# Performance work log

Hardware: AMD Instinct MI355X
Metric: run time of the kernel (lower is better)

The kernel has to match this reference:

```python
import jax, jax.numpy as jnp
import numpy as np

MARGIN = 0.5
ALPHA = 1.0
BETA = 0.5
TEMP = 0.07
TEMP_MIN = 0.01
TEMP_MAX = 0.5
STEP = 1  # step_count after first forward (buffer starts at 0, incremented before use)
WARMUP = 1000


def _l2norm(x):
    return x / jnp.maximum(jnp.linalg.norm(x, axis=1, keepdims=True), 1e-12)


def _adaptive_temp(std):
    return jnp.clip(TEMP * (1.0 + std), TEMP_MIN, TEMP_MAX)


def setup_inputs() -> dict:
    key = jax.random.key(0)
    k1, k2, k3, k4, k5 = jax.random.split(key, 5)
    B, D, C, P = 4096, 1024, 1000, 2000
    return {
        "features": jax.random.normal(k1, (B, D), dtype=jnp.float32),
        "cur_proto": jax.random.normal(k2, (C, D), dtype=jnp.float32),
        "prev_proto": jax.random.normal(k3, (P, D), dtype=jnp.float32),
        "labels": jax.random.randint(k4, (B,), 0, C, dtype=jnp.int32),
        "prev_proto_labels": jax.random.randint(k5, (P,), 0, C, dtype=jnp.int32),
    }


def reference(features, cur_proto, prev_proto, labels, prev_proto_labels):
    # With randn protos, proto norms ~ sqrt(D)=32 in (1e-3, 100), so valid_mask
    # is all-True; the per-sample torch loop vectorizes exactly.
    f = _l2norm(features)          # [B, D]
    cp = _l2norm(cur_proto)        # [C, D]

    # --- positive alignment: cosine_embedding_loss(target=1) = mean(1 - cos) ---
    pos_cos = jnp.sum(f * cp[labels], axis=1)       # [B]
    pos_loss = jnp.mean(1.0 - pos_cos)

    # --- curriculum weight at step 1 ---
    w = 0.1 + 0.9 * (STEP / WARMUP)
    curr_beta = BETA * w

    # --- intra-domain InfoNCE vs current prototypes (smooth_loss branch) ---
    # all_sims per sample is a permutation of the full row of sims -> std invariant
    sims = f @ cp.T                                  # [B, C]
    std = jnp.std(sims, axis=1, ddof=1)              # torch.std is unbiased
    temp = _adaptive_temp(std)[:, None]              # [B, 1]
    logits = sims / temp
    pos_logit = jnp.take_along_axis(logits, labels[:, None], axis=1)[:, 0]
    infonce = jax.scipy.special.logsumexp(logits, axis=1) - pos_logit
    loss_neg_total = jnp.mean(infonce)

    # --- cross-domain vs previous-domain prototypes of different class ---
    pp = _l2norm(prev_proto)                         # [P, D]
    csims = f @ pp.T                                 # [B, P]
    m = (prev_proto_labels[None, :] != labels[:, None]).astype(f.dtype)  # [B, P]
    n = jnp.sum(m, axis=1)                           # [B], >1 w.h.p.
    mean = jnp.sum(csims * m, axis=1) / n
    var = jnp.sum(m * (csims - mean[:, None]) ** 2, axis=1) / (n - 1.0)
    ctemp = (_adaptive_temp(jnp.sqrt(var)) * 2.0)[:, None]
    clogits = jnp.where(m > 0, csims / ctemp, -jnp.inf)
    cross = jax.scipy.special.logsumexp(clogits, axis=1)  # [B]
    loss_neg_total = loss_neg_total + 0.3 * jnp.mean(cross)

    total = ALPHA * pos_loss + curr_beta * loss_neg_total
    return total
```

## Files before the change

### kernel.cpp

```cpp
#include <hip/hip_runtime.h>
#include <hip/hip_bf16.h>
#include <math.h>

typedef __attribute__((ext_vector_type(4))) float floatx4;
typedef __attribute__((ext_vector_type(8))) __bf16 bf16x8;

#define B_ROWS 4096
#define D_DIM  1024
#define C_CUR  1000
#define P_PREV 2000
#define C_PAD  1024
#define P_PAD  2048
#define N_TOT  (C_PAD + P_PAD)

#define LDS_BARRIER() asm volatile("s_waitcnt lgkmcnt(0)\n\ts_barrier" ::: "memory")

__device__ __forceinline__ float wave_sum(float v) {
#pragma unroll
  for (int o = 32; o > 0; o >>= 1) v += __shfl_xor(v, o, 64);
  return v;
}
__device__ __forceinline__ float wave_max(float v) {
#pragma unroll
  for (int o = 32; o > 0; o >>= 1) v = fmaxf(v, __shfl_xor(v, o, 64));
  return v;
}

__global__ __launch_bounds__(256) void norm_all_kernel(
    const float* __restrict__ features, const float* __restrict__ cur_proto,
    const float* __restrict__ prev_proto, __hip_bfloat16* __restrict__ fn,
    __hip_bfloat16* __restrict__ proto) {
  const int wv = threadIdx.x >> 6, lane = threadIdx.x & 63;
  const int r = blockIdx.x * 4 + wv;
  const float* src;
  unsigned short* dst;
  bool valid;
  if (r < B_ROWS) {
    src = features + (size_t)r * D_DIM;
    dst = (unsigned short*)fn + (size_t)r * D_DIM;
    valid = true;
  } else if (r < B_ROWS + C_PAD) {
    const int rr = r - B_ROWS;
    src = cur_proto + (size_t)rr * D_DIM;
    dst = (unsigned short*)proto + (size_t)rr * D_DIM;
    valid = rr < C_CUR;
  } else {
    const int rr = r - B_ROWS - C_PAD;
    src = prev_proto + (size_t)rr * D_DIM;
    dst = (unsigned short*)proto + (size_t)(C_PAD + rr) * D_DIM;
    valid = rr < P_PREV;
  }
  if (!valid) {
    ushort4 z = {0, 0, 0, 0};
#pragma unroll
    for (int k = 0; k < 4; ++k) *(ushort4*)(dst + lane * 4 + k * 256) = z;
    return;
  }
  float4 v[4];
  float ss = 0.f;
#pragma unroll
  for (int k = 0; k < 4; ++k) {
    v[k] = *(const float4*)(src + lane * 4 + k * 256);
    ss += v[k].x * v[k].x + v[k].y * v[k].y + v[k].z * v[k].z + v[k].w * v[k].w;
  }
  ss = wave_sum(ss);
  const float inv = 1.0f / fmaxf(sqrtf(ss), 1e-12f);
#pragma unroll
  for (int k = 0; k < 4; ++k) {
    __hip_bfloat16 h0 = __float2bfloat16(v[k].x * inv);
    __hip_bfloat16 h1 = __float2bfloat16(v[k].y * inv);
    __hip_bfloat16 h2 = __float2bfloat16(v[k].z * inv);
    __hip_bfloat16 h3 = __float2bfloat16(v[k].w * inv);
    ushort4 u;
    u.x = *(unsigned short*)&h0;
    u.y = *(unsigned short*)&h1;
    u.z = *(unsigned short*)&h2;
    u.w = *(unsigned short*)&h3;
    *(ushort4*)(dst + lane * 4 + k * 256) = u;
  }
}

#define TM    128
#define BK    32
#define KITER (D_DIM / BK)

__global__ __launch_bounds__(256) void gemm_bf16_kernel(
    const __hip_bfloat16* __restrict__ A,
    const __hip_bfloat16* __restrict__ Bm,
    __hip_bfloat16* __restrict__ Cm) {
  __shared__ alignas(16) unsigned short lA[2][TM * BK];
  __shared__ alignas(16) unsigned short lB[2][TM * BK];
  const int t = threadIdx.x;
  const int bm = blockIdx.y, bn = blockIdx.x;
  const unsigned short* Ag = (const unsigned short*)A + (size_t)bm * TM * D_DIM;
  const unsigned short* Bg = (const unsigned short*)Bm + (size_t)bn * TM * D_DIM;

  const int lane = t & 63, wv = t >> 6;
  const int wm = (wv >> 1) * 64, wn = (wv & 1) * 64;
  const int quad = lane >> 4, l16 = lane & 15;

  const int qa = wv * 64 + lane;
  const int row_a = qa >> 2, ko = (lane & 3) * 8;
  const unsigned short* a0p = Ag + (size_t)row_a * D_DIM + ko;
  const unsigned short* a1p = Ag + (size_t)(row_a + 64) * D_DIM + ko;
  const unsigned short* b0p = Bg + (size_t)row_a * D_DIM + ko;
  const unsigned short* b1p = Bg + (size_t)(row_a + 64) * D_DIM + ko;
  const int wr0 = qa * 8;
  const int wr1 = qa * 8 + 2048;

  floatx4 acc[4][4] = {};

  float4 a0 = *(const float4*)(a0p);
  float4 a1 = *(const float4*)(a1p);
  float4 b0 = *(const float4*)(b0p);
  float4 b1 = *(const float4*)(b1p);
  *(float4*)(lA[0] + wr0) = a0;
  *(float4*)(lA[0] + wr1) = a1;
  *(float4*)(lB[0] + wr0) = b0;
  *(float4*)(lB[0] + wr1) = b1;
  a0 = *(const float4*)(a0p + BK);
  a1 = *(const float4*)(a1p + BK);
  b0 = *(const float4*)(b0p + BK);
  b1 = *(const float4*)(b1p + BK);
  LDS_BARRIER();

#pragma unroll 2
  for (int i = 0; i < KITER; ++i) {
    const int p = i & 1;
    if (i < KITER - 1) {
      *(float4*)(lA[1 - p] + wr0) = a0;
      *(float4*)(lA[1 - p] + wr1) = a1;
      *(float4*)(lB[1 - p] + wr0) = b0;
      *(float4*)(lB[1 - p] + wr1) = b1;
      const int nk = (i + 2 < KITER) ? (i + 2) * BK : (KITER - 1) * BK;
      a0 = *(const float4*)(a0p + nk);
      a1 = *(const float4*)(a1p + nk);
      b0 = *(const float4*)(b0p + nk);
      b1 = *(const float4*)(b1p + nk);
    }
    bf16x8 af[4], bfr[4];
#pragma unroll
    for (int x = 0; x < 4; ++x)
      af[x] = *(const bf16x8*)(lA[p] + (wm + x * 16 + l16) * BK + quad * 8);
#pragma unroll
    for (int y = 0; y < 4; ++y)
      bfr[y] = *(const bf16x8*)(lB[p] + (wn + y * 16 + l16) * BK + quad * 8);
#pragma unroll
    for (int x = 0; x < 4; ++x)
#pragma unroll
      for (int y = 0; y < 4; ++y)
        acc[x][y] = __builtin_amdgcn_mfma_f32_16x16x32_bf16(af[x], bfr[y], acc[x][y], 0, 0, 0);
    LDS_BARRIER();
  }

  unsigned short* Cu = (unsigned short*)Cm;
#pragma unroll
  for (int x = 0; x < 4; ++x)
#pragma unroll
    for (int y = 0; y < 4; ++y)
#pragma unroll
      for (int r = 0; r < 4; ++r) {
        const int row = bm * TM + wm + x * 16 + quad * 4 + r;
        const int col = bn * TM + wn + y * 16 + l16;
        __hip_bfloat16 h = __float2bfloat16(acc[x][y][r]);
        Cu[(size_t)row * N_TOT + col] = *(unsigned short*)&h;
      }
}

__global__ __launch_bounds__(256) void row_reduce_kernel(
    const __hip_bfloat16* __restrict__ sims, const int* __restrict__ labels,
    const int* __restrict__ ppl,
    float* __restrict__ pos_o, float* __restrict__ inf_o, float* __restrict__ crs_o) {
  const int wv = threadIdx.x >> 6, lane = threadIdx.x & 63;
  const int b = blockIdx.x * 4 + wv;
  const unsigned short* row = (const unsigned short*)sims + (size_t)b * N_TOT;
  const int lab = labels[b];

  {
    const int i1 = 512 + lane * 8;
    float vi[16];
    bf16x8 u0 = *(const bf16x8*)(row + lane * 8);
    bf16x8 u1 = *(const bf16x8*)(row + i1);
#pragma unroll
    for (int j = 0; j < 8; ++j) { vi[j] = (float)u0[j]; vi[8 + j] = (float)u1[j]; }
    float sum = 0.f, sq = 0.f, mx = -1e30f;
#pragma unroll
    for (int j = 0; j < 8; ++j) {
      float v = vi[j];
      sum += v; sq += v * v; mx = fmaxf(mx, v);
    }
#pragma unroll
    for (int j = 0; j < 8; ++j) {
      if (i1 + j < C_CUR) { float v = vi[8 + j]; sum += v; sq += v * v; mx = fmaxf(mx, v); }
    }
    sum = wave_sum(sum); sq = wave_sum(sq); mx = wave_max(mx);
    const float var = (sq - sum * sum / (float)C_CUR) / (float)(C_CUR - 1);
    const float sd = sqrtf(fmaxf(var, 0.f));
    const float temp = fminf(fmaxf(0.07f * (1.f + sd), 0.01f), 0.5f);
    const float it = 1.f / temp;
    float se = 0.f;
#pragma unroll
    for (int j = 0; j < 8; ++j) se += __expf((vi[j] - mx) * it);
#pragma unroll
    for (int j = 0; j < 8; ++j)
      if (i1 + j < C_CUR) se += __expf((vi[8 + j] - mx) * it);
    se = wave_sum(se);
    if (lane == 0) {
      __hip_bfloat16 hs;
      *(unsigned short*)&hs = row[lab];
      const float slab = __bfloat162float(hs);
      pos_o[b] = 1.f - slab;
      inf_o[b] = mx * it + logf(se) - slab * it;
    }
  }

  {
    const unsigned short* crow = row + C_PAD;
    float vc[32];
    unsigned mask = 0;
    float sum = 0.f, sq = 0.f, mx = -1e30f;
    int cnt = 0;
#pragma unroll
    for (int k = 0; k < 4; ++k) {
      const int base = k * 512 + lane * 8;
      bf16x8 u = *(const bf16x8*)(crow + base);
#pragma unroll
      for (int j = 0; j < 8; ++j) vc[k * 8 + j] = (float)u[j];
      if (base < P_PREV) {
        int4 p0 = *(const int4*)(ppl + base);
        int4 p1 = *(const int4*)(ppl + base + 4);
        const int pl[8] = {p0.x, p0.y, p0.z, p0.w, p1.x, p1.y, p1.z, p1.w};
#pragma unroll
        for (int j = 0; j < 8; ++j) {
          if (pl[j] != lab) {
            mask |= 1u << (k * 8 + j);
            float v = vc[k * 8 + j];
            sum += v; sq += v * v; mx = fmaxf(mx, v); ++cnt;
          }
        }
      }
    }
    sum = wave_sum(sum); sq = wave_sum(sq); mx = wave_max(mx);
    const float n = wave_sum((float)cnt);
    const float var = (sq - sum * sum / n) / (n - 1.f);
    const float sd = sqrtf(fmaxf(var, 0.f));
    const float ct = 2.f * fminf(fmaxf(0.07f * (1.f + sd), 0.01f), 0.5f);
    const float it = 1.f / ct;
    float se = 0.f;
#pragma unroll
    for (int e = 0; e < 32; ++e)
      if ((mask >> e) & 1u) se += __expf((vc[e] - mx) * it);
    se = wave_sum(se);
    if (lane == 0) crs_o[b] = mx * it + logf(se);
  }
}

__global__ __launch_bounds__(1024) void final_reduce_kernel(
    const float* __restrict__ pos_o, const float* __restrict__ inf_o,
    const float* __restrict__ crs_o, float* __restrict__ out) {
  const int t = threadIdx.x;
  __shared__ float sA[1024], sB[1024], sC[1024];
  float a = 0.f, bb = 0.f, c = 0.f;
  for (int i = t; i < B_ROWS; i += 1024) {
    a += pos_o[i]; bb += inf_o[i]; c += crs_o[i];
  }
  sA[t] = a; sB[t] = bb; sC[t] = c;
  __syncthreads();
  for (int o = 512; o > 0; o >>= 1) {
    if (t < o) { sA[t] += sA[t + o]; sB[t] += sB[t + o]; sC[t] += sC[t + o]; }
    __syncthreads();
  }
  if (t == 0) {
    const float invB = 1.f / (float)B_ROWS;
    const float pos = sA[0] * invB;
    const float neg = sB[0] * invB + 0.3f * sC[0] * invB;
    const float curr_beta = 0.5f * (0.1f + 0.9f * (1.0f / 1000.0f));
    out[0] = pos + curr_beta * neg;
  }
}

extern "C" void kernel_launch(void* const* d_in, const int* in_sizes, int n_in,
                              void* d_out, int out_size, void* d_ws, size_t ws_size,
                              hipStream_t stream) {
  const float* features   = (const float*)d_in[0];
  const float* cur_proto  = (const float*)d_in[1];
  const float* prev_proto = (const float*)d_in[2];
  const int*   labels     = (const int*)d_in[3];
  const int*   ppl        = (const int*)d_in[4];

  char* w = (char*)d_ws;
  __hip_bfloat16* fn    = (__hip_bfloat16*)w;
  __hip_bfloat16* proto = (__hip_bfloat16*)(w + (size_t)8 * 1024 * 1024);
  __hip_bfloat16* sims  = (__hip_bfloat16*)(w + (size_t)14 * 1024 * 1024);
  char* tail = w + (size_t)14 * 1024 * 1024 + (size_t)B_ROWS * N_TOT * 2;
  float* pos_o = (float*)tail;
  float* inf_o = pos_o + B_ROWS;
  float* crs_o = inf_o + B_ROWS;

  norm_all_kernel<<<(B_ROWS + C_PAD + P_PAD) / 4, 256, 0, stream>>>(
      features, cur_proto, prev_proto, fn, proto);

  dim3 grid(N_TOT / TM, B_ROWS / TM);
  gemm_bf16_kernel<<<grid, 256, 0, stream>>>(fn, proto, sims);

  row_reduce_kernel<<<B_ROWS / 4, 256, 0, stream>>>(sims, labels, ppl, pos_o, inf_o, crs_o);
  final_reduce_kernel<<<1, 1024, 0, stream>>>(pos_o, inf_o, crs_o, (float*)d_out);
}
```

Baseline: 127.8 us.

## Quantize normalized operands to FP8 e4m3 and use FP8 MFMA GEMM

Normalized features and prototypes are now stored as FP8 e4m3 bytes using a hand-written software converter, and the similarity GEMM switches to the fp8 16x16x32 MFMA with padded LDS rows. This halves the operand bytes read by the GEMM and the workspace they occupy, and uses the higher-throughput FP8 matrix path. The cost is a large precision loss on the cosine similarities, which feed exponentials divided by small temperatures and could push the loss outside tolerance. The per-element software conversion also adds ALU work to the normalization kernel.

```diff
diff --git a/kernel.cpp b/kernel.cpp
--- a/kernel.cpp
+++ b/kernel.cpp
@@ -26,130 +26,127 @@
   return v;
 }
 
+__device__ __forceinline__ unsigned char f32_to_e4m3(float x) {
+  unsigned u = __float_as_uint(x);
+  unsigned s = (u >> 24) & 0x80u;
+  float a = fabsf(x);
+  if (a < 0.015625f) {
+    int q = (int)rintf(a * 512.0f);
+    return (unsigned char)(s | (unsigned)q);
+  }
+  unsigned au = u & 0x7fffffffu;
+  unsigned r = au + 0x0007ffffu + ((au >> 20) & 1u);
+  int e = (int)(r >> 23) - 127;
+  unsigned m = (r >> 20) & 7u;
+  return (unsigned char)(s | ((unsigned)(e + 7) << 3) | m);
+}
+
 __global__ __launch_bounds__(256) void norm_all_kernel(
     const float* __restrict__ features, const float* __restrict__ cur_proto,
-    const float* __restrict__ prev_proto, __hip_bfloat16* __restrict__ fn,
-    __hip_bfloat16* __restrict__ proto) {
+    const float* __restrict__ prev_proto, unsigned char* __restrict__ fn,
+    unsigned char* __restrict__ proto) {
   const int wv = threadIdx.x >> 6, lane = threadIdx.x & 63;
   const int r = blockIdx.x * 4 + wv;
   const float* src;
-  unsigned short* dst;
+  unsigned char* dst;
   bool valid;
   if (r < B_ROWS) {
     src = features + (size_t)r * D_DIM;
-    dst = (unsigned short*)fn + (size_t)r * D_DIM;
+    dst = fn + (size_t)r * D_DIM;
     valid = true;
   } else if (r < B_ROWS + C_PAD) {
     const int rr = r - B_ROWS;
     src = cur_proto + (size_t)rr * D_DIM;
-    dst = (unsigned short*)proto + (size_t)rr * D_DIM;
+    dst = proto + (size_t)rr * D_DIM;
     valid = rr < C_CUR;
   } else {
     const int rr = r - B_ROWS - C_PAD;
     src = prev_proto + (size_t)rr * D_DIM;
-    dst = (unsigned short*)proto + (size_t)(C_PAD + rr) * D_DIM;
+    dst = proto + (size_t)(C_PAD + rr) * D_DIM;
     valid = rr < P_PREV;
   }
   if (!valid) {
-    ushort4 z = {0, 0, 0, 0};
-#pragma unroll
-    for (int k = 0; k < 4; ++k) *(ushort4*)(dst + lane * 4 + k * 256) = z;
+    uint4 z = {0, 0, 0, 0};
+    *(uint4*)(dst + lane * 16) = z;
     return;
   }
   float4 v[4];
   float ss = 0.f;
 #pragma unroll
   for (int k = 0; k < 4; ++k) {
-    v[k] = *(const float4*)(src + lane * 4 + k * 256);
+    v[k] = *(const float4*)(src + lane * 16 + k * 4);
     ss += v[k].x * v[k].x + v[k].y * v[k].y + v[k].z * v[k].z + v[k].w * v[k].w;
   }
   ss = wave_sum(ss);
   const float inv = 1.0f / fmaxf(sqrtf(ss), 1e-12f);
+  union { unsigned char b[16]; uint4 q; } o;
 #pragma unroll
   for (int k = 0; k < 4; ++k) {
-    __hip_bfloat16 h0 = __float2bfloat16(v[k].x * inv);
-    __hip_bfloat16 h1 = __float2bfloat16(v[k].y * inv);
-    __hip_bfloat16 h2 = __float2bfloat16(v[k].z * inv);
-    __hip_bfloat16 h3 = __float2bfloat16(v[k].w * inv);
-    ushort4 u;
-    u.x = *(unsigned short*)&h0;
-    u.y = *(unsigned short*)&h1;
-    u.z = *(unsigned short*)&h2;
-    u.w = *(unsigned short*)&h3;
-    *(ushort4*)(dst + lane * 4 + k * 256) = u;
-  }
+    o.b[k * 4 + 0] = f32_to_e4m3(v[k].x * inv);
+    o.b[k * 4 + 1] = f32_to_e4m3(v[k].y * inv);
+    o.b[k * 4 + 2] = f32_to_e4m3(v[k].z * inv);
+    o.b[k * 4 + 3] = f32_to_e4m3(v[k].w * inv);
+  }
+  *(uint4*)(dst + lane * 16) = o.q;
 }
 
 #define TM    128
 #define BK    32
+#define LSTRB 48
 #define KITER (D_DIM / BK)
 
-__global__ __launch_bounds__(256) void gemm_bf16_kernel(
-    const __hip_bfloat16* __restrict__ A,
-    const __hip_bfloat16* __restrict__ Bm,
+__global__ __launch_bounds__(256) void gemm_fp8_kernel(
+    const unsigned char* __restrict__ A,
+    const unsigned char* __restrict__ Bm,
     __hip_bfloat16* __restrict__ Cm) {
-  __shared__ alignas(16) unsigned short lA[2][TM * BK];
-  __shared__ alignas(16) unsigned short lB[2][TM * BK];
+  __shared__ alignas(16) unsigned char lA[2][TM * LSTRB];
+  __shared__ alignas(16) unsigned char lB[2][TM * LSTRB];
   const int t = threadIdx.x;
   const int bm = blockIdx.y, bn = blockIdx.x;
-  const unsigned short* Ag = (const unsigned short*)A + (size_t)bm * TM * D_DIM;
-  const unsigned short* Bg = (const unsigned short*)Bm + (size_t)bn * TM * D_DIM;
+  const unsigned char* Ag = A + (size_t)bm * TM * D_DIM;
+  const unsigned char* Bg = Bm + (size_t)bn * TM * D_DIM;
 
   const int lane = t & 63, wv = t >> 6;
   const int wm = (wv >> 1) * 64, wn = (wv & 1) * 64;
   const int quad = lane >> 4, l16 = lane & 15;
 
-  const int qa = wv * 64 + lane;
-  const int row_a = qa >> 2, ko = (lane & 3) * 8;
-  const unsigned short* a0p = Ag + (size_t)row_a * D_DIM + ko;
-  const unsigned short* a1p = Ag + (size_t)(row_a + 64) * D_DIM + ko;
-  const unsigned short* b0p = Bg + (size_t)row_a * D_DIM + ko;
-  const unsigned short* b1p = Bg + (size_t)(row_a + 64) * D_DIM + ko;
-  const int wr0 = qa * 8;
-  const int wr1 = qa * 8 + 2048;
+  const int srow = t >> 1, shalf = (t & 1) * 16;
+  const unsigned char* ap = Ag + (size_t)srow * D_DIM + shalf;
+  const unsigned char* bp = Bg + (size_t)srow * D_DIM + shalf;
+  const int wroff = srow * LSTRB + shalf;
 
   floatx4 acc[4][4] = {};
 
-  float4 a0 = *(const float4*)(a0p);
-  float4 a1 = *(const float4*)(a1p);
-  float4 b0 = *(const float4*)(b0p);
-  float4 b1 = *(const float4*)(b1p);
-  *(float4*)(lA[0] + wr0) = a0;
-  *(float4*)(lA[0] + wr1) = a1;
-  *(float4*)(lB[0] + wr0) = b0;
-  *(float4*)(lB[0] + wr1) = b1;
-  a0 = *(const float4*)(a0p + BK);
-  a1 = *(const float4*)(a1p + BK);
-  b0 = *(const float4*)(b0p + BK);
-  b1 = *(const float4*)(b1p + BK);
+  float4 a0 = *(const float4*)(ap);
+  float4 b0 = *(const float4*)(bp);
+  *(float4*)(lA[0] + wroff) = a0;
+  *(float4*)(lB[0] + wroff) = b0;
+  a0 = *(const float4*)(ap + BK);
+  b0 = *(const float4*)(bp + BK);
   LDS_BARRIER();
 
 #pragma unroll 2
   for (int i = 0; i < KITER; ++i) {
     const int p = i & 1;
     if (i < KITER - 1) {
-      *(float4*)(lA[1 - p] + wr0) = a0;
-      *(float4*)(lA[1 - p] + wr1) = a1;
-      *(float4*)(lB[1 - p] + wr0) = b0;
-      *(float4*)(lB[1 - p] + wr1) = b1;
+      *(float4*)(lA[1 - p] + wroff) = a0;
+      *(float4*)(lB[1 - p] + wroff) = b0;
       const int nk = (i + 2 < KITER) ? (i + 2) * BK : (KITER - 1) * BK;
-      a0 = *(const float4*)(a0p + nk);
-      a1 = *(const float4*)(a1p + nk);
-      b0 = *(const float4*)(b0p + nk);
-      b1 = *(const float4*)(b1p + nk);
-    }
-    bf16x8 af[4], bfr[4];
+      a0 = *(const float4*)(ap + nk);
+      b0 = *(const float4*)(bp + nk);
+    }
+    long long af[4], bfr[4];
 #pragma unroll
     for (int x = 0; x < 4; ++x)
-      af[x] = *(const bf16x8*)(lA[p] + (wm + x * 16 + l16) * BK + quad * 8);
+      af[x] = *(const long long*)(lA[p] + (wm + x * 16 + l16) * LSTRB + quad * 8);
 #pragma unroll
     for (int y = 0; y < 4; ++y)
-      bfr[y] = *(const bf16x8*)(lB[p] + (wn + y * 16 + l16) * BK + quad * 8);
+      bfr[y] = *(const long long*)(lB[p] + (wn + y * 16 + l16) * LSTRB + quad * 8);
 #pragma unroll
     for (int x = 0; x < 4; ++x)
 #pragma unroll
       for (int y = 0; y < 4; ++y)
-        acc[x][y] = __builtin_amdgcn_mfma_f32_16x16x32_bf16(af[x], bfr[y], acc[x][y], 0, 0, 0);
+        acc[x][y] = __builtin_amdgcn_mfma_f32_16x16x32_fp8_fp8(af[x], bfr[y], acc[x][y], 0, 0, 0);
     LDS_BARRIER();
   }
 
@@ -289,10 +286,10 @@
   const int*   ppl        = (const int*)d_in[4];
 
   char* w = (char*)d_ws;
-  __hip_bfloat16* fn    = (__hip_bfloat16*)w;
-  __hip_bfloat16* proto = (__hip_bfloat16*)(w + (size_t)8 * 1024 * 1024);
-  __hip_bfloat16* sims  = (__hip_bfloat16*)(w + (size_t)14 * 1024 * 1024);
-  char* tail = w + (size_t)14 * 1024 * 1024 + (size_t)B_ROWS * N_TOT * 2;
+  unsigned char* fn    = (unsigned char*)w;
+  unsigned char* proto = (unsigned char*)(w + (size_t)4 * 1024 * 1024);
+  __hip_bfloat16* sims = (__hip_bfloat16*)(w + (size_t)8 * 1024 * 1024);
+  char* tail = w + (size_t)8 * 1024 * 1024 + (size_t)B_ROWS * N_TOT * 2;
   float* pos_o = (float*)tail;
   float* inf_o = pos_o + B_ROWS;
   float* crs_o = inf_o + B_ROWS;
@@ -301,7 +298,7 @@
       features, cur_proto, prev_proto, fn, proto);
 
   dim3 grid(N_TOT / TM, B_ROWS / TM);
-  gemm_bf16_kernel<<<grid, 256, 0, stream>>>(fn, proto, sims);
+  gemm_fp8_kernel<<<grid, 256, 0, stream>>>(fn, proto, sims);
 
   row_reduce_kernel<<<B_ROWS / 4, 256, 0, stream>>>(sims, labels, ppl, pos_o, inf_o, crs_o);
   final_reduce_kernel<<<1, 1024, 0, stream>>>(pos_o, inf_o, crs_o, (float*)d_out);
```

New measurement: 123.0 us. 1.04x faster.
